# Kernel optimization log

Measured on AMD Instinct MI355X. Metric: run time of the kernel, lower is better.

Reference implementation:

```python
import jax, jax.numpy as jnp
import numpy as np

B, S, LATENT = 256, 64, 20
U_DIM = LATENT // 5            # 4
T_HID, T_DEPTH = 20, 4         # treatment MLP
D_HID, D_DEPTH = 4 * LATENT, 4 # drift MLP (80 hidden)
T_LEN = 41
DT = 0.05
SIGMA, THETA, MU = 0.5, 1.0, 0.0
N = B * S
DIM_AUG = LATENT + 2           # latent + logqp + Tx


def _mlp(x, w_in, b_in, w_h, b_h, w_out, b_out, act):
    # input layer always ReLU (MLPSimple), hidden layers use `act`
    h = jax.nn.relu(x @ w_in.T + b_in)
    for i in range(w_h.shape[0]):
        h = act(h @ w_h[i].T + b_h[i])
    return h @ w_out.T + b_out


def setup_inputs() -> dict:
    key = jax.random.key(0)
    ks = jax.random.split(key, 20)

    def lin(k, out_d, in_d):
        bound = 1.0 / np.sqrt(in_d)
        return jax.random.uniform(k, (out_d, in_d), jnp.float32, -bound, bound)

    def bias(k, out_d, in_d):
        bound = 1.0 / np.sqrt(in_d)
        return jax.random.uniform(k, (out_d,), jnp.float32, -bound, bound)

    return {
        "z_SDE": jax.random.normal(ks[0], (B, S, LATENT), jnp.float32),
        "t": jnp.arange(T_LEN, dtype=jnp.float32) * DT,
        "Tx": jax.random.uniform(ks[1], (B,), jnp.float32),
        "noise": jax.random.normal(ks[2], (T_LEN - 1, N, DIM_AUG), jnp.float32),
        # treatment MLP: 1 -> 20 (ReLU) -> [20->20 ReLU]x4 -> 4
        "tw_in": lin(ks[3], T_HID, 1),
        "tb_in": bias(ks[4], T_HID, 1),
        "tw_h": jnp.stack([lin(jax.random.fold_in(ks[5], i), T_HID, T_HID) for i in range(T_DEPTH)]),
        "tb_h": jnp.stack([bias(jax.random.fold_in(ks[6], i), T_HID, T_HID) for i in range(T_DEPTH)]),
        "tw_out": lin(ks[7], U_DIM, T_HID),
        "tb_out": bias(ks[8], U_DIM, T_HID),
        # drift MLP: 24 -> 80 (ReLU) -> [80->80 Tanh]x4 -> 20
        "dw_in": lin(ks[9], D_HID, LATENT + U_DIM),
        "db_in": bias(ks[10], D_HID, LATENT + U_DIM),
        "dw_h": jnp.stack([lin(jax.random.fold_in(ks[11], i), D_HID, D_HID) for i in range(D_DEPTH)]),
        "db_h": jnp.stack([bias(jax.random.fold_in(ks[12], i), D_HID, D_HID) for i in range(D_DEPTH)]),
        "dw_out": lin(ks[13], LATENT, D_HID),
        "db_out": bias(ks[14], LATENT, D_HID),
    }


def reference(z_SDE, t, Tx, noise, tw_in, tb_in, tw_h, tb_h, tw_out, tb_out,
              dw_in, db_in, dw_h, db_h, dw_out, db_out):
    # build augmented initial state: [z, logqp0=0, Tx]  -> [N, DIM_AUG]
    Tx_rep = jnp.broadcast_to(Tx[:, None, None], (B, S, 1))
    aug_y0 = jnp.concatenate(
        [z_SDE, jnp.zeros((B, S, 1), z_SDE.dtype), Tx_rep.astype(z_SDE.dtype)], axis=-1
    ).reshape(N, DIM_AUG)

    dt = t[1] - t[0]           # 0.05, aligned with euler dt
    sqrt_dt = jnp.sqrt(dt)
    # diagonal diffusion: sigma on latent dims, 0 on (logqp, Tx) aug dims
    g_diag = jnp.concatenate([jnp.full((LATENT,), SIGMA, jnp.float32), jnp.zeros((2,), jnp.float32)])

    def f_aug(ti, y_aug):
        T_ = y_aug[:, -1]                     # treatment indicator
        y = y_aug[:, :LATENT]
        t_col = jnp.broadcast_to(ti, (N, 1)).astype(y.dtype)
        u = _mlp(t_col, tw_in, tb_in, tw_h, tb_h, tw_out, tb_out, jax.nn.relu)
        u_t = u * T_[:, None]
        h = THETA * (MU - y)                  # prior drift
        f = _mlp(jnp.concatenate([y, u_t], axis=-1), dw_in, db_in, dw_h, db_h, dw_out, db_out, jnp.tanh) - h
        # _stable_division(f - h, g); g = sigma = 0.5 > eps so plain division
        uu = (f - h) / SIGMA
        f_logqp = 0.5 * jnp.sum(uu * uu, axis=1, keepdims=True)
        return jnp.concatenate([f, f_logqp, jnp.zeros_like(f_logqp)], axis=1)

    def step(y, inp):
        ti, dW = inp
        y_new = y + f_aug(ti, y) * dt + g_diag[None, :] * (dW * sqrt_dt)
        return y_new, y_new

    _, ys_rest = jax.lax.scan(step, aug_y0, (t[:-1], noise))
    aug_ys = jnp.concatenate([aug_y0[None], ys_rest], axis=0)   # [T, N, DIM_AUG]
    # faithful to source: raw reshape of [T, N, dim] into [B, S, T, dim]
    aug_ys = aug_ys.reshape(-1, S, T_LEN, DIM_AUG)
    ys = aug_ys[:, :, :, :-2]
    logqp = aug_ys[:, :, -1, -2]
    return ys, logqp
```

## Files before the change

kernel.cpp:

```cpp
#include <hip/hip_runtime.h>
#include <math.h>
#include <stdint.h>

#define NPART 16384
#define NSTEP 40
#define DIMA  22
#define OUT0_ELEMS 13434880
#define TRAJ_OFF   160

typedef __attribute__((ext_vector_type(8))) short short8;
typedef __attribute__((ext_vector_type(4))) float floatx4;
typedef __attribute__((ext_vector_type(4))) int   intx4;
typedef __attribute__((ext_vector_type(2))) int   intx2;

union V4 { intx4 i; short8 s; floatx4 f; };

#define AIN_B   0
#define AH_B    5120
#define AOUT_B  56320
#define U_B     61440
#define LDS_BYTES 62080
#define STAGE_DW  15360

__device__ __forceinline__ uint32_t pk2(float a0, float a1) {
    uint32_t r;
    asm("v_cvt_pk_bf16_f32 %0, %1, %2" : "=v"(r) : "v"(a0), "v"(a1));
    return r;
}
__device__ __forceinline__ float fast_tanh(float x) {
    float e = __expf(2.0f * x);
    return 1.0f - 2.0f * __builtin_amdgcn_rcpf(e + 1.0f);
}

__global__ __launch_bounds__(256, 1) void sde_mfma(
    const float* __restrict__ z,      const float* __restrict__ t_arr,
    const float* __restrict__ Tx,     const float* __restrict__ noise,
    const float* __restrict__ dw_in,  const float* __restrict__ db_in,
    const float* __restrict__ dw_h,   const float* __restrict__ db_h,
    const float* __restrict__ dw_out, const float* __restrict__ db_out,
    const float* __restrict__ tw_in,  const float* __restrict__ tb_in,
    const float* __restrict__ tw_h,   const float* __restrict__ tb_h,
    const float* __restrict__ tw_out, const float* __restrict__ tb_out,
    float* __restrict__ out0,         float* __restrict__ traj)
{
    __shared__ __align__(16) uint8_t lds[LDS_BYTES];
    const int tid = threadIdx.x;

    for (int di = tid; di < STAGE_DW; di += 256) {
        uint32_t val = 0u;
        if (di < 1280) {
            int r = di & 255, lane = r >> 2, w = r & 3;
            int m = lane & 15, q = lane >> 4, mt = di >> 8;
            int f = -1;
            if (w < 2)            f = 4 * q + 2 * w;
            else if (q == 0)      f = 16 + 2 * (w - 2);
            else if (q == 1)      f = 20 + 2 * (w - 2);
            if (f >= 0)               val = pk2(dw_in[(mt * 16 + m) * 24 + f],
                                                dw_in[(mt * 16 + m) * 24 + f + 1]);
            else if (q == 2 && w == 2) val = pk2(db_in[mt * 16 + m], 0.f);
        } else if (di < 14080) {
            int q2 = di - 1280, g = q2 / 640, r = q2 % 640;
            int l = g / 5, mt = g % 5;
            int lane, f;
            if (r < 512) {
                int kt = r >> 8, rr = r & 255, w = rr & 3;
                lane = rr >> 2;
                f = 16 * (2 * kt + (w >> 1)) + 4 * (lane >> 4) + 2 * (w & 1);
            } else {
                int rr = r - 512, d = rr & 1;
                lane = rr >> 1;
                f = 64 + 4 * (lane >> 4) + 2 * d;
            }
            int m = lane & 15;
            val = pk2(dw_h[l * 6400 + (mt * 16 + m) * 80 + f],
                      dw_h[l * 6400 + (mt * 16 + m) * 80 + f + 1]);
        } else {
            int q2 = di - 14080, mt = q2 / 640, r = q2 % 640;
            int lane, f;
            if (r < 512) {
                int kt = r >> 8, rr = r & 255, w = rr & 3;
                lane = rr >> 2;
                f = 16 * (2 * kt + (w >> 1)) + 4 * (lane >> 4) + 2 * (w & 1);
            } else {
                int rr = r - 512, d = rr & 1;
                lane = rr >> 1;
                f = 64 + 4 * (lane >> 4) + 2 * d;
            }
            int m = mt * 16 + (lane & 15);
            if (m < 20) val = pk2(dw_out[m * 80 + f], dw_out[m * 80 + f + 1]);
        }
        ((uint32_t*)lds)[di] = val;
    }
    if (tid < NSTEP) {
        float ti = t_arr[tid];
        float hh[20], h2[20];
        #pragma unroll
        for (int j = 0; j < 20; j++) {
            float v = tw_in[j] * ti + tb_in[j];
            hh[j] = v > 0.f ? v : 0.f;
        }
        #pragma unroll
        for (int l = 0; l < 4; l++) {
            #pragma unroll
            for (int j = 0; j < 20; j++) {
                float a = tb_h[l * 20 + j];
                #pragma unroll
                for (int k = 0; k < 20; k++) a += tw_h[(l * 20 + j) * 20 + k] * hh[k];
                h2[j] = a > 0.f ? a : 0.f;
            }
            #pragma unroll
            for (int j = 0; j < 20; j++) hh[j] = h2[j];
        }
        #pragma unroll
        for (int c = 0; c < 4; c++) {
            float a = tb_out[c];
            #pragma unroll
            for (int k = 0; k < 20; k++) a += tw_out[c * 20 + k] * hh[k];
            ((float*)(lds + U_B))[tid * 4 + c] = a;
        }
    }

    const int lane = tid & 63;
    const int n15  = lane & 15;
    const int quad = lane >> 4;
    const int wv   = tid >> 6;
    const int n    = blockIdx.x * 64 + wv * 16 + n15;
    const float Txb = Tx[blockIdx.x];
    const float dtv = t_arr[1] - t_arr[0];
    const float sdt = sqrtf(dtv);

    __syncthreads();

    V4 aIn[5];
    #pragma unroll
    for (int mt = 0; mt < 5; mt++)
        aIn[mt].i = *(const intx4*)(lds + AIN_B + mt * 1024 + lane * 16);

    V4 aH0[20], aH1[20], aH2[20];
    #pragma unroll
    for (int l = 0; l < 4; l++) {
        #pragma unroll
        for (int mt = 0; mt < 5; mt++) {
            const int g = l * 5 + mt;
            const uint8_t* grp = lds + AH_B + (size_t)g * 2560;
            aH0[g].i = *(const intx4*)(grp + lane * 16);
            aH1[g].i = *(const intx4*)(grp + 1024 + lane * 16);
            intx2 h2 = *(const intx2*)(grp + 2048 + lane * 8);
            uint32_t bd = (quad == 0) ? pk2(db_h[l * 80 + mt * 16 + n15], 0.f) : 0u;
            aH2[g].i = (intx4){h2[0], h2[1], (int)bd, 0};
        }
    }

    V4 aO0[2], aO1[2], aO2[2];
    #pragma unroll
    for (int mt = 0; mt < 2; mt++) {
        const uint8_t* grp = lds + AOUT_B + (size_t)mt * 2560;
        aO0[mt].i = *(const intx4*)(grp + lane * 16);
        aO1[mt].i = *(const intx4*)(grp + 1024 + lane * 16);
        intx2 h2 = *(const intx2*)(grp + 2048 + lane * 8);
        int m = mt * 16 + n15;
        uint32_t bd = (quad == 0 && m < 20) ? pk2(db_out[m], 0.f) : 0u;
        aO2[mt].i = (intx4){h2[0], h2[1], (int)bd, 0};
    }

    const floatx4 zf = {0.f, 0.f, 0.f, 0.f};

    float y0[4], y1[4] = {0.f, 0.f, 0.f, 0.f};
    {
        floatx4 zv = *(const floatx4*)(z + (size_t)n * 20 + quad * 4);
        #pragma unroll
        for (int r = 0; r < 4; r++) y0[r] = zv[r];
        *(floatx4*)(out0 + (size_t)n * 20 + quad * 4) = zv;
        if (quad == 0) {
            floatx4 z2 = *(const floatx4*)(z + (size_t)n * 20 + 16);
            #pragma unroll
            for (int r = 0; r < 4; r++) y1[r] = z2[r];
            *(floatx4*)(out0 + (size_t)n * 20 + 16) = z2;
            traj[n] = 0.f;
        }
    }

    double lq = 0.0;
    for (int i = 0; i < NSTEP; i++) {
        size_t nbase = ((size_t)i * NPART + n) * DIMA;
        floatx4 dW0 = *(const floatx4*)(noise + nbase + quad * 4);
        floatx4 dW1 = {0.f, 0.f, 0.f, 0.f};
        if (quad == 0) dW1 = *(const floatx4*)(noise + nbase + 16);

        const floatx4 uv = *(const floatx4*)((const float*)(lds + U_B) + i * 4);
        float ut0 = uv[0] * Txb, ut1 = uv[1] * Txb;
        float ut2 = uv[2] * Txb, ut3 = uv[3] * Txb;

        V4 bin;
        bin.i[0] = pk2(y0[0], y0[1]);
        bin.i[1] = pk2(y0[2], y0[3]);
        if (quad == 0)      { bin.i[2] = pk2(y1[0], y1[1]); bin.i[3] = pk2(y1[2], y1[3]); }
        else if (quad == 1) { bin.i[2] = pk2(ut0, ut1);     bin.i[3] = pk2(ut2, ut3); }
        else if (quad == 2) { bin.i[2] = 0x00003F80;        bin.i[3] = 0; }
        else                { bin.i[2] = 0;                 bin.i[3] = 0; }

        floatx4 acc[5];
        #pragma unroll
        for (int mt = 0; mt < 5; mt++)
            acc[mt] = __builtin_amdgcn_mfma_f32_16x16x32_bf16(aIn[mt].s, bin.s, zf, 0, 0, 0);
        uint32_t pkA[5][2];
        #pragma unroll
        for (int mt = 0; mt < 5; mt++) {
            pkA[mt][0] = pk2(fmaxf(acc[mt][0], 0.f), fmaxf(acc[mt][1], 0.f));
            pkA[mt][1] = pk2(fmaxf(acc[mt][2], 0.f), fmaxf(acc[mt][3], 0.f));
        }

        #pragma unroll
        for (int l = 0; l < 4; l++) {
            V4 b0, b1, b2;
            b0.i = (intx4){(int)pkA[0][0], (int)pkA[0][1], (int)pkA[1][0], (int)pkA[1][1]};
            b1.i = (intx4){(int)pkA[2][0], (int)pkA[2][1], (int)pkA[3][0], (int)pkA[3][1]};
            b2.i = (intx4){(int)pkA[4][0], (int)pkA[4][1], 0x00003F80, 0};
            #pragma unroll
            for (int mt = 0; mt < 5; mt++) {
                const int g = l * 5 + mt;
                floatx4 c;
                c = __builtin_amdgcn_mfma_f32_16x16x32_bf16(aH0[g].s, b0.s, zf, 0, 0, 0);
                c = __builtin_amdgcn_mfma_f32_16x16x32_bf16(aH1[g].s, b1.s, c, 0, 0, 0);
                c = __builtin_amdgcn_mfma_f32_16x16x32_bf16(aH2[g].s, b2.s, c, 0, 0, 0);
                acc[mt] = c;
            }
            #pragma unroll
            for (int mt = 0; mt < 5; mt++) {
                pkA[mt][0] = pk2(fast_tanh(acc[mt][0]), fast_tanh(acc[mt][1]));
                pkA[mt][1] = pk2(fast_tanh(acc[mt][2]), fast_tanh(acc[mt][3]));
            }
        }

        V4 b0, b1, b2;
        b0.i = (intx4){(int)pkA[0][0], (int)pkA[0][1], (int)pkA[1][0], (int)pkA[1][1]};
        b1.i = (intx4){(int)pkA[2][0], (int)pkA[2][1], (int)pkA[3][0], (int)pkA[3][1]};
        b2.i = (intx4){(int)pkA[4][0], (int)pkA[4][1], 0x00003F80, 0};
        floatx4 oacc[2];
        #pragma unroll
        for (int mt = 0; mt < 2; mt++) {
            floatx4 c;
            c = __builtin_amdgcn_mfma_f32_16x16x32_bf16(aO0[mt].s, b0.s, zf, 0, 0, 0);
            c = __builtin_amdgcn_mfma_f32_16x16x32_bf16(aO1[mt].s, b1.s, c, 0, 0, 0);
            oacc[mt] = __builtin_amdgcn_mfma_f32_16x16x32_bf16(aO2[mt].s, b2.s, c, 0, 0, 0);
        }

        float part = 0.f;
        size_t obase = ((size_t)(i + 1) * NPART + n) * 20;
        floatx4 st;
        #pragma unroll
        for (int r = 0; r < 4; r++) {
            float o = oacc[0][r];
            float y = y0[r];
            float f = o + y;
            float uu = 2.f * o + 4.f * y;
            part += uu * uu;
            y0[r] = y + f * dtv + (0.5f * sdt) * dW0[r];
            st[r] = y0[r];
        }
        *(floatx4*)(out0 + obase + quad * 4) = st;
        if (quad == 0) {
            floatx4 st2;
            #pragma unroll
            for (int r = 0; r < 4; r++) {
                float o = oacc[1][r];
                float y = y1[r];
                float f = o + y;
                float uu = 2.f * o + 4.f * y;
                part += uu * uu;
                y1[r] = y + f * dtv + (0.5f * sdt) * dW1[r];
                st2[r] = y1[r];
            }
            *(floatx4*)(out0 + obase + 16) = st2;
        }
        part += __shfl_xor(part, 16);
        part += __shfl_xor(part, 32);
        lq += 0.5 * (double)part * (double)dtv;
        if (quad == 0) traj[(size_t)(i + 1) * NPART + n] = (float)lq;
    }
}

__global__ void gather_logqp(const float* __restrict__ traj, float* __restrict__ out1) {
    int i = blockIdx.x * 256 + threadIdx.x;
    if (i < NPART) out1[i] = traj[(size_t)41 * i + 40];
}

extern "C" void kernel_launch(void* const* d_in, const int* in_sizes, int n_in,
                              void* d_out, int out_size, void* d_ws, size_t ws_size,
                              hipStream_t stream) {
    const float* z      = (const float*)d_in[0];
    const float* t_arr  = (const float*)d_in[1];
    const float* Tx     = (const float*)d_in[2];
    const float* noise  = (const float*)d_in[3];
    const float* tw_in  = (const float*)d_in[4];
    const float* tb_in  = (const float*)d_in[5];
    const float* tw_h   = (const float*)d_in[6];
    const float* tb_h   = (const float*)d_in[7];
    const float* tw_out = (const float*)d_in[8];
    const float* tb_out = (const float*)d_in[9];
    const float* dw_in  = (const float*)d_in[10];
    const float* db_in  = (const float*)d_in[11];
    const float* dw_h   = (const float*)d_in[12];
    const float* db_h   = (const float*)d_in[13];
    const float* dw_out = (const float*)d_in[14];
    const float* db_out = (const float*)d_in[15];

    float* wsf  = (float*)d_ws;
    float* traj = wsf + TRAJ_OFF;
    float* out0 = (float*)d_out;
    float* out1 = out0 + OUT0_ELEMS;

    hipLaunchKernelGGL(sde_mfma, dim3(256), dim3(256), 0, stream,
                       z, t_arr, Tx, noise, dw_in, db_in, dw_h, db_h,
                       dw_out, db_out, tw_in, tb_in, tw_h, tb_h, tw_out, tb_out,
                       out0, traj);
    hipLaunchKernelGGL(gather_logqp, dim3(64), dim3(256), 0, stream, traj, out1);
}
```

Before: 259.7 us.

## Process two particle chains per wave to interleave independent MFMA sequences

Each wave now advances two independent 16-particle groups, and the grid is halved to 128 blocks. The two groups' MFMA chains are interleaved so the serial dependency latency of the MLP layers is hidden. The log-qp accumulator also moves from double to float. The cost is higher register pressure and half as many blocks, which leaves many of the GPU's CUs idle.

```diff
diff --git a/kernel.cpp b/kernel.cpp
--- a/kernel.cpp
+++ b/kernel.cpp
@@ -124,10 +124,11 @@
     const int n15  = lane & 15;
     const int quad = lane >> 4;
     const int wv   = tid >> 6;
-    const int n    = blockIdx.x * 64 + wv * 16 + n15;
-    const float Txb = Tx[blockIdx.x];
+    const int nb   = blockIdx.x * 128 + wv * 32 + n15;
+    const float Txb = Tx[blockIdx.x * 2 + (wv >> 1)];
     const float dtv = t_arr[1] - t_arr[0];
     const float sdt = sqrtf(dtv);
+    const float hsdt = 0.5f * sdt;
 
     __syncthreads();
 
@@ -165,118 +166,152 @@
 
     const floatx4 zf = {0.f, 0.f, 0.f, 0.f};
 
-    float y0[4], y1[4] = {0.f, 0.f, 0.f, 0.f};
-    {
+    float y0[2][4], y1[2][4];
+    #pragma unroll
+    for (int c = 0; c < 2; c++) {
+        const int n = nb + c * 16;
         floatx4 zv = *(const floatx4*)(z + (size_t)n * 20 + quad * 4);
         #pragma unroll
-        for (int r = 0; r < 4; r++) y0[r] = zv[r];
+        for (int r = 0; r < 4; r++) { y0[c][r] = zv[r]; y1[c][r] = 0.f; }
         *(floatx4*)(out0 + (size_t)n * 20 + quad * 4) = zv;
         if (quad == 0) {
             floatx4 z2 = *(const floatx4*)(z + (size_t)n * 20 + 16);
             #pragma unroll
-            for (int r = 0; r < 4; r++) y1[r] = z2[r];
+            for (int r = 0; r < 4; r++) y1[c][r] = z2[r];
             *(floatx4*)(out0 + (size_t)n * 20 + 16) = z2;
             traj[n] = 0.f;
         }
     }
 
-    double lq = 0.0;
+    float lq[2] = {0.f, 0.f};
     for (int i = 0; i < NSTEP; i++) {
-        size_t nbase = ((size_t)i * NPART + n) * DIMA;
-        floatx4 dW0 = *(const floatx4*)(noise + nbase + quad * 4);
-        floatx4 dW1 = {0.f, 0.f, 0.f, 0.f};
-        if (quad == 0) dW1 = *(const floatx4*)(noise + nbase + 16);
+        floatx4 dW0[2], dW1[2];
+        #pragma unroll
+        for (int c = 0; c < 2; c++) {
+            size_t nbase = ((size_t)i * NPART + (nb + c * 16)) * DIMA;
+            dW0[c] = *(const floatx4*)(noise + nbase + quad * 4);
+            dW1[c] = zf;
+            if (quad == 0) dW1[c] = *(const floatx4*)(noise + nbase + 16);
+        }
 
         const floatx4 uv = *(const floatx4*)((const float*)(lds + U_B) + i * 4);
         float ut0 = uv[0] * Txb, ut1 = uv[1] * Txb;
         float ut2 = uv[2] * Txb, ut3 = uv[3] * Txb;
-
-        V4 bin;
-        bin.i[0] = pk2(y0[0], y0[1]);
-        bin.i[1] = pk2(y0[2], y0[3]);
-        if (quad == 0)      { bin.i[2] = pk2(y1[0], y1[1]); bin.i[3] = pk2(y1[2], y1[3]); }
-        else if (quad == 1) { bin.i[2] = pk2(ut0, ut1);     bin.i[3] = pk2(ut2, ut3); }
-        else if (quad == 2) { bin.i[2] = 0x00003F80;        bin.i[3] = 0; }
-        else                { bin.i[2] = 0;                 bin.i[3] = 0; }
-
-        floatx4 acc[5];
-        #pragma unroll
-        for (int mt = 0; mt < 5; mt++)
-            acc[mt] = __builtin_amdgcn_mfma_f32_16x16x32_bf16(aIn[mt].s, bin.s, zf, 0, 0, 0);
-        uint32_t pkA[5][2];
+        uint32_t utp0 = pk2(ut0, ut1), utp1 = pk2(ut2, ut3);
+
+        V4 bin[2];
+        #pragma unroll
+        for (int c = 0; c < 2; c++) {
+            bin[c].i[0] = pk2(y0[c][0], y0[c][1]);
+            bin[c].i[1] = pk2(y0[c][2], y0[c][3]);
+            if (quad == 0)      { bin[c].i[2] = pk2(y1[c][0], y1[c][1]); bin[c].i[3] = pk2(y1[c][2], y1[c][3]); }
+            else if (quad == 1) { bin[c].i[2] = (int)utp0;               bin[c].i[3] = (int)utp1; }
+            else if (quad == 2) { bin[c].i[2] = 0x00003F80;              bin[c].i[3] = 0; }
+            else                { bin[c].i[2] = 0;                       bin[c].i[3] = 0; }
+        }
+
+        floatx4 acc[2][5];
         #pragma unroll
         for (int mt = 0; mt < 5; mt++) {
-            pkA[mt][0] = pk2(fmaxf(acc[mt][0], 0.f), fmaxf(acc[mt][1], 0.f));
-            pkA[mt][1] = pk2(fmaxf(acc[mt][2], 0.f), fmaxf(acc[mt][3], 0.f));
+            acc[0][mt] = __builtin_amdgcn_mfma_f32_16x16x32_bf16(aIn[mt].s, bin[0].s, zf, 0, 0, 0);
+            acc[1][mt] = __builtin_amdgcn_mfma_f32_16x16x32_bf16(aIn[mt].s, bin[1].s, zf, 0, 0, 0);
+        }
+        uint32_t pkA[2][5][2];
+        #pragma unroll
+        for (int mt = 0; mt < 5; mt++) {
+            #pragma unroll
+            for (int c = 0; c < 2; c++) {
+                pkA[c][mt][0] = pk2(fmaxf(acc[c][mt][0], 0.f), fmaxf(acc[c][mt][1], 0.f));
+                pkA[c][mt][1] = pk2(fmaxf(acc[c][mt][2], 0.f), fmaxf(acc[c][mt][3], 0.f));
+            }
         }
 
         #pragma unroll
         for (int l = 0; l < 4; l++) {
-            V4 b0, b1, b2;
-            b0.i = (intx4){(int)pkA[0][0], (int)pkA[0][1], (int)pkA[1][0], (int)pkA[1][1]};
-            b1.i = (intx4){(int)pkA[2][0], (int)pkA[2][1], (int)pkA[3][0], (int)pkA[3][1]};
-            b2.i = (intx4){(int)pkA[4][0], (int)pkA[4][1], 0x00003F80, 0};
+            V4 b0[2], b1[2], b2[2];
+            #pragma unroll
+            for (int c = 0; c < 2; c++) {
+                b0[c].i = (intx4){(int)pkA[c][0][0], (int)pkA[c][0][1], (int)pkA[c][1][0], (int)pkA[c][1][1]};
+                b1[c].i = (intx4){(int)pkA[c][2][0], (int)pkA[c][2][1], (int)pkA[c][3][0], (int)pkA[c][3][1]};
+                b2[c].i = (intx4){(int)pkA[c][4][0], (int)pkA[c][4][1], 0x00003F80, 0};
+            }
             #pragma unroll
             for (int mt = 0; mt < 5; mt++) {
                 const int g = l * 5 + mt;
-                floatx4 c;
-                c = __builtin_amdgcn_mfma_f32_16x16x32_bf16(aH0[g].s, b0.s, zf, 0, 0, 0);
-                c = __builtin_amdgcn_mfma_f32_16x16x32_bf16(aH1[g].s, b1.s, c, 0, 0, 0);
-                c = __builtin_amdgcn_mfma_f32_16x16x32_bf16(aH2[g].s, b2.s, c, 0, 0, 0);
-                acc[mt] = c;
+                #pragma unroll
+                for (int c = 0; c < 2; c++) {
+                    floatx4 cc;
+                    cc = __builtin_amdgcn_mfma_f32_16x16x32_bf16(aH0[g].s, b0[c].s, zf, 0, 0, 0);
+                    cc = __builtin_amdgcn_mfma_f32_16x16x32_bf16(aH1[g].s, b1[c].s, cc, 0, 0, 0);
+                    cc = __builtin_amdgcn_mfma_f32_16x16x32_bf16(aH2[g].s, b2[c].s, cc, 0, 0, 0);
+                    acc[c][mt] = cc;
+                }
             }
             #pragma unroll
             for (int mt = 0; mt < 5; mt++) {
-                pkA[mt][0] = pk2(fast_tanh(acc[mt][0]), fast_tanh(acc[mt][1]));
-                pkA[mt][1] = pk2(fast_tanh(acc[mt][2]), fast_tanh(acc[mt][3]));
-            }
-        }
-
-        V4 b0, b1, b2;
-        b0.i = (intx4){(int)pkA[0][0], (int)pkA[0][1], (int)pkA[1][0], (int)pkA[1][1]};
-        b1.i = (intx4){(int)pkA[2][0], (int)pkA[2][1], (int)pkA[3][0], (int)pkA[3][1]};
-        b2.i = (intx4){(int)pkA[4][0], (int)pkA[4][1], 0x00003F80, 0};
-        floatx4 oacc[2];
+                #pragma unroll
+                for (int c = 0; c < 2; c++) {
+                    pkA[c][mt][0] = pk2(fast_tanh(acc[c][mt][0]), fast_tanh(acc[c][mt][1]));
+                    pkA[c][mt][1] = pk2(fast_tanh(acc[c][mt][2]), fast_tanh(acc[c][mt][3]));
+                }
+            }
+        }
+
+        V4 b0[2], b1[2], b2[2];
+        #pragma unroll
+        for (int c = 0; c < 2; c++) {
+            b0[c].i = (intx4){(int)pkA[c][0][0], (int)pkA[c][0][1], (int)pkA[c][1][0], (int)pkA[c][1][1]};
+            b1[c].i = (intx4){(int)pkA[c][2][0], (int)pkA[c][2][1], (int)pkA[c][3][0], (int)pkA[c][3][1]};
+            b2[c].i = (intx4){(int)pkA[c][4][0], (int)pkA[c][4][1], 0x00003F80, 0};
+        }
+        floatx4 oacc[2][2];
         #pragma unroll
         for (int mt = 0; mt < 2; mt++) {
-            floatx4 c;
-            c = __builtin_amdgcn_mfma_f32_16x16x32_bf16(aO0[mt].s, b0.s, zf, 0, 0, 0);
-            c = __builtin_amdgcn_mfma_f32_16x16x32_bf16(aO1[mt].s, b1.s, c, 0, 0, 0);
-            oacc[mt] = __builtin_amdgcn_mfma_f32_16x16x32_bf16(aO2[mt].s, b2.s, c, 0, 0, 0);
-        }
-
-        float part = 0.f;
-        size_t obase = ((size_t)(i + 1) * NPART + n) * 20;
-        floatx4 st;
-        #pragma unroll
-        for (int r = 0; r < 4; r++) {
-            float o = oacc[0][r];
-            float y = y0[r];
-            float f = o + y;
-            float uu = 2.f * o + 4.f * y;
-            part += uu * uu;
-            y0[r] = y + f * dtv + (0.5f * sdt) * dW0[r];
-            st[r] = y0[r];
-        }
-        *(floatx4*)(out0 + obase + quad * 4) = st;
-        if (quad == 0) {
-            floatx4 st2;
+            #pragma unroll
+            for (int c = 0; c < 2; c++) {
+                floatx4 cc;
+                cc = __builtin_amdgcn_mfma_f32_16x16x32_bf16(aO0[mt].s, b0[c].s, zf, 0, 0, 0);
+                cc = __builtin_amdgcn_mfma_f32_16x16x32_bf16(aO1[mt].s, b1[c].s, cc, 0, 0, 0);
+                oacc[c][mt] = __builtin_amdgcn_mfma_f32_16x16x32_bf16(aO2[mt].s, b2[c].s, cc, 0, 0, 0);
+            }
+        }
+
+        #pragma unroll
+        for (int c = 0; c < 2; c++) {
+            const int n = nb + c * 16;
+            float part = 0.f;
+            size_t obase = ((size_t)(i + 1) * NPART + n) * 20;
+            floatx4 st;
             #pragma unroll
             for (int r = 0; r < 4; r++) {
-                float o = oacc[1][r];
-                float y = y1[r];
+                float o = oacc[c][0][r];
+                float y = y0[c][r];
                 float f = o + y;
                 float uu = 2.f * o + 4.f * y;
                 part += uu * uu;
-                y1[r] = y + f * dtv + (0.5f * sdt) * dW1[r];
-                st2[r] = y1[r];
-            }
-            *(floatx4*)(out0 + obase + 16) = st2;
-        }
-        part += __shfl_xor(part, 16);
-        part += __shfl_xor(part, 32);
-        lq += 0.5 * (double)part * (double)dtv;
-        if (quad == 0) traj[(size_t)(i + 1) * NPART + n] = (float)lq;
+                y0[c][r] = y + f * dtv + hsdt * dW0[c][r];
+                st[r] = y0[c][r];
+            }
+            *(floatx4*)(out0 + obase + quad * 4) = st;
+            if (quad == 0) {
+                floatx4 st2;
+                #pragma unroll
+                for (int r = 0; r < 4; r++) {
+                    float o = oacc[c][1][r];
+                    float y = y1[c][r];
+                    float f = o + y;
+                    float uu = 2.f * o + 4.f * y;
+                    part += uu * uu;
+                    y1[c][r] = y + f * dtv + hsdt * dW1[c][r];
+                    st2[r] = y1[c][r];
+                }
+                *(floatx4*)(out0 + obase + 16) = st2;
+            }
+            part += __shfl_xor(part, 16);
+            part += __shfl_xor(part, 32);
+            lq[c] += 0.5f * part * dtv;
+            if (quad == 0) traj[(size_t)(i + 1) * NPART + n] = lq[c];
+        }
     }
 }
 
@@ -310,7 +345,7 @@
     float* out0 = (float*)d_out;
     float* out1 = out0 + OUT0_ELEMS;
 
-    hipLaunchKernelGGL(sde_mfma, dim3(256), dim3(256), 0, stream,
+    hipLaunchKernelGGL(sde_mfma, dim3(128), dim3(256), 0, stream,
                        z, t_arr, Tx, noise, dw_in, db_in, dw_h, db_h,
                        dw_out, db_out, tw_in, tb_in, tw_h, tb_h, tw_out, tb_out,
                        out0, traj);
```

Result: slower. 346.7 us (+33.5%).
